# Kernel tuning notes

Hardware: AMD Instinct MI355X
Metric: run time of the kernel (lower is better)

The kernel has to match this reference:

```python
import jax, jax.numpy as jnp
import numpy as np


def setup_inputs() -> dict:
    key = jax.random.key(0)
    ks = jax.random.split(key, 5)
    B, T, I, H = 64, 512, 1024, 1024
    s = 1.0 / np.sqrt(H)
    return {
        "x": jax.random.normal(ks[0], (B, T, I), dtype=jnp.float32),
        "w_ih": jax.random.normal(ks[1], (4 * H, I), dtype=jnp.float32) * s,
        "b_ih": jax.random.normal(ks[2], (4 * H,), dtype=jnp.float32) * s,
        "w_hh": jax.random.normal(ks[3], (4 * H, H), dtype=jnp.float32) * s,
        "b_hh": jax.random.normal(ks[4], (4 * H,), dtype=jnp.float32) * s,
    }


def _lstm(x, w_ih, b_ih, w_hh, b_hh):
    B, T, _ = x.shape
    H = w_hh.shape[1]
    # Precompute input projections for all timesteps: [T, B, 4H]
    gx = jnp.einsum("bti,gi->tbg", x, w_ih) + b_ih
    h0 = jnp.zeros((B, H), dtype=x.dtype)
    c0 = jnp.zeros((B, H), dtype=x.dtype)

    def step(carry, g_x):
        h, c = carry
        gates = g_x + h @ w_hh.T + b_hh  # [B, 4H]
        i_lin, f_lin, g_lin, o_lin = jnp.split(gates, 4, axis=-1)
        i = jax.nn.sigmoid(i_lin)
        f = jax.nn.sigmoid(f_lin)
        g = jnp.tanh(g_lin)
        o = jax.nn.sigmoid(o_lin)
        c = f * c + i * g
        h = o * jnp.tanh(c)
        return (h, c), h

    (hT, cT), hs = jax.lax.scan(step, (h0, c0), gx)
    output = jnp.transpose(hs, (1, 0, 2))  # [B, T, H]
    hn = hT[None, :, :]  # [1, B, H]
    cn = cT[None, :, :]
    return output, hn, cn


def reference(x, w_ih, b_ih, w_hh, b_hh):
    return _lstm(x, w_ih, b_ih, w_hh, b_hh)
```

## Files before the change

kernel.cpp:

```cpp
#include <hip/hip_runtime.h>
#include <hip/hip_bf16.h>

#define Bv 64
#define Tv 512
#define Iv 1024
#define Hv 1024
#define G4v 4096
#define BH (Bv * Hv)
#define NHB 64
#define NXB 128
#define NBLK (NHB + NXB)
#define DEPTH 8
#define FSTR 16

typedef __attribute__((ext_vector_type(8))) short bf16x8;
typedef __attribute__((ext_vector_type(4))) float f32x4;

#define LOADC(p)    __hip_atomic_load((p), __ATOMIC_RELAXED, __HIP_MEMORY_SCOPE_AGENT)
#define STOREC(p,v) __hip_atomic_store((p), (v), __ATOMIC_RELAXED, __HIP_MEMORY_SCOPE_AGENT)

__device__ __forceinline__ float sigmoid_f(float v) { return 1.f / (1.f + __expf(-v)); }
__device__ __forceinline__ float tanh_f(float v) { return 1.f - 2.f / (__expf(2.f * v) + 1.f); }

__global__ void prep(const float* __restrict__ w_ih, const float* __restrict__ w_hh,
                     const float* __restrict__ b_ih, const float* __restrict__ b_hh,
                     __hip_bfloat16* __restrict__ wbih, __hip_bfloat16* __restrict__ wbhh,
                     float* __restrict__ bias, __hip_bfloat16* __restrict__ hbuf,
                     unsigned* __restrict__ hflag, unsigned* __restrict__ xflag) {
  unsigned i = blockIdx.x * 256u + threadIdx.x;
  wbih[i] = __float2bfloat16(w_ih[i]);
  wbhh[i] = __float2bfloat16(w_hh[i]);
  if (i < (unsigned)G4v) bias[i] = b_ih[i] + b_hh[i];
  if (i < 2u * BH) hbuf[i] = __float2bfloat16(0.f);
  if (i < (unsigned)(NHB * FSTR)) hflag[i] = 0u;
  if (i < (unsigned)(NXB * FSTR)) xflag[i] = 0u;
}

#define LOAD4(buf, cc)                                                  \
  _Pragma("unroll")                                                     \
  for (int j = 0; j < 4; ++j) {                                         \
    buf[2 * j]     = LOADC(hq + ((cc) * 4 + j) * 8);                    \
    buf[2 * j + 1] = LOADC(hq + ((cc) * 4 + j) * 8 + 1);                \
  }
#define MFMA4(buf, cc)                                                  \
  _Pragma("unroll")                                                     \
  for (int j = 0; j < 4; ++j) {                                         \
    int k0 = (((cc) * 4 + j) << 5) + lk;                                \
    union { unsigned long long q[2]; bf16x8 v; } ua;                    \
    ua.q[0] = buf[2 * j]; ua.q[1] = buf[2 * j + 1];                     \
    _Pragma("unroll")                                                   \
    for (int nf = 0; nf < 4; ++nf) {                                    \
      int n = nf * 16 + lrow;                                           \
      unsigned byt = (unsigned)((n << 11) + (k0 << 1)) ^ ((unsigned)(n & 7) << 4); \
      bf16x8 b = *(const bf16x8*)(&lds[byt]);                           \
      acc[nf] = __builtin_amdgcn_mfma_f32_16x16x32_bf16(ua.v, b, acc[nf], 0, 0, 0); \
    }                                                                   \
  }

__global__ void __launch_bounds__(256, 1) lstm_main(
    const float* __restrict__ x,
    const __hip_bfloat16* __restrict__ wbih,
    const __hip_bfloat16* __restrict__ wbhh,
    const float* __restrict__ bias,
    __hip_bfloat16* __restrict__ hbuf,
    float* __restrict__ xg,
    float* __restrict__ out,
    unsigned* __restrict__ hflag,
    unsigned* __restrict__ xflag,
    int ring)
{
  extern __shared__ char lds[];
  float* gbuf = (float*)(lds + 131072);

  const int bid  = blockIdx.x;
  const bool is_h = (bid < NHB);
  const int tid  = threadIdx.x;
  const int lane = tid & 63;
  const int wave = tid >> 6;
  const int lrow = lane & 15;
  const int lkg  = lane >> 4;
  const int lk   = lkg * 8;

  const int wg = is_h ? bid : ((bid - NHB) >> 1);
  const int rh = is_h ? 0 : ((bid - NHB) & 1);

  {
    const __hip_bfloat16* wsrc = is_h ? wbhh : wbih;
    for (int c = tid; c < 8192; c += 256) {
      int n   = c >> 7;
      int k16 = c & 127;
      int gc  = ((n >> 4) << 10) + (wg << 4) + (n & 15);
      uint4 v = *(const uint4*)(wsrc + ((size_t)gc << 10) + (k16 << 3));
      unsigned byt = (unsigned)((n << 11) + (k16 << 4)) ^ ((unsigned)(n & 7) << 4);
      *(uint4*)(&lds[byt]) = v;
    }
  }
  __syncthreads();

  if (!is_h) {
    const int j  = bid - NHB;
    const int wr = wave & 1;
    const int wc = wave >> 1;
    const int arow = rh * 32 + wr * 16 + lrow;
    const float* xa = x + (size_t)arow * (Tv * Iv) + lk;

    for (int t = 0; t < Tv; ++t) {
      if (t >= DEPTH) {
        if (wave == 0) {
          const unsigned tgt = (unsigned)(t - DEPTH + 1);
          for (;;) {
            unsigned hf = LOADC(&hflag[lane * FSTR]);
            if (__all(hf >= tgt)) break;
            __builtin_amdgcn_s_sleep(4);
          }
        }
        __syncthreads();
        asm volatile("" ::: "memory");
      }
      f32x4 acc[2];
      acc[0] = f32x4{0.f,0.f,0.f,0.f}; acc[1] = f32x4{0.f,0.f,0.f,0.f};
      const float* xt = xa + (size_t)t * Iv;
      #pragma unroll 4
      for (int ks = 0; ks < 32; ++ks) {
        int k0 = (ks << 5) + lk;
        float4 f0 = *(const float4*)(xt + (ks << 5));
        float4 f1 = *(const float4*)(xt + (ks << 5) + 4);
        union { __hip_bfloat16 e[8]; bf16x8 v; } u;
        u.e[0] = __float2bfloat16(f0.x); u.e[1] = __float2bfloat16(f0.y);
        u.e[2] = __float2bfloat16(f0.z); u.e[3] = __float2bfloat16(f0.w);
        u.e[4] = __float2bfloat16(f1.x); u.e[5] = __float2bfloat16(f1.y);
        u.e[6] = __float2bfloat16(f1.z); u.e[7] = __float2bfloat16(f1.w);
        bf16x8 b0, b1;
        {
          int n = wc * 32 + lrow;
          unsigned byt = (unsigned)((n << 11) + (k0 << 1)) ^ ((unsigned)(n & 7) << 4);
          b0 = *(const bf16x8*)(&lds[byt]);
          n += 16;
          byt = (unsigned)((n << 11) + (k0 << 1)) ^ ((unsigned)(n & 7) << 4);
          b1 = *(const bf16x8*)(&lds[byt]);
        }
        acc[0] = __builtin_amdgcn_mfma_f32_16x16x32_bf16(u.v, b0, acc[0], 0, 0, 0);
        acc[1] = __builtin_amdgcn_mfma_f32_16x16x32_bf16(u.v, b1, acc[1], 0, 0, 0);
      }
      float* dst = xg + (size_t)(t & (DEPTH - 1)) * (Bv * G4v);
      for (int nf = 0; nf < 2; ++nf) {
        int gc  = (wc * 2 + nf) * 1024 + (wg << 4) + lrow;
        int row = rh * 32 + wr * 16 + (lkg << 2);
        for (int r = 0; r < 4; ++r)
          STOREC(&dst[(size_t)(row + r) * G4v + gc], acc[nf][r]);
      }
      asm volatile("s_waitcnt vmcnt(0)" ::: "memory");
      __syncthreads();
      if (tid == 0) STOREC(&xflag[j * FSTR], (unsigned)(t + 1));
      __syncthreads();
    }
    return;
  }

  const int eb  = tid >> 2;
  const int ec0 = (tid & 3) << 2;
  float c_state[4] = {0.f, 0.f, 0.f, 0.f};
  float biasv[16];
  for (int g = 0; g < 4; ++g)
    for (int jj = 0; jj < 4; ++jj)
      biasv[g * 4 + jj] = bias[(g << 10) + (wg << 4) + ec0 + jj];

  const int ar = wave * 16 + lrow;

  for (int t = 0; t < Tv; ++t) {
    if (wave == 0) {
      const unsigned ht = (unsigned)t, xtg = (unsigned)(t + 1);
      const unsigned* xf = &xflag[(2 * wg + (lane & 1)) * FSTR];
      for (;;) {
        unsigned hf = LOADC(&hflag[lane * FSTR]);
        unsigned xv = LOADC(xf);
        if (__all(hf >= ht && xv >= xtg)) break;
        __builtin_amdgcn_s_sleep(1);
      }
    }
    __syncthreads();
    asm volatile("" ::: "memory");
    float xgv[16];
    {
      const unsigned long long* xq = (const unsigned long long*)
          (xg + (size_t)(t & (DEPTH - 1)) * (Bv * G4v) + (size_t)eb * G4v + (wg << 4) + ec0);
      #pragma unroll
      for (int g = 0; g < 4; ++g) {
        union { unsigned long long q[2]; float f[4]; } ux;
        ux.q[0] = LOADC(xq + g * 512);
        ux.q[1] = LOADC(xq + g * 512 + 1);
        xgv[g * 4 + 0] = ux.f[0]; xgv[g * 4 + 1] = ux.f[1];
        xgv[g * 4 + 2] = ux.f[2]; xgv[g * 4 + 3] = ux.f[3];
      }
    }
    f32x4 acc[4];
    for (int nf = 0; nf < 4; ++nf) acc[nf] = f32x4{0.f,0.f,0.f,0.f};
    if (ring) {
      const __hip_bfloat16* hp2 = hbuf + (size_t)t * BH;
      const char* hrow = (const char*)hp2 + ((size_t)ar << 11) + (lkg << 4);
      bf16x8 aqv[32];
      #pragma unroll
      for (int ks = 0; ks < 32; ++ks)
        aqv[ks] = *(const bf16x8*)(hrow + (ks << 6));
      #pragma unroll
      for (int ks = 0; ks < 32; ++ks) {
        int k0 = (ks << 5) + lk;
        #pragma unroll
        for (int nf = 0; nf < 4; ++nf) {
          int n = nf * 16 + lrow;
          unsigned byt = (unsigned)((n << 11) + (k0 << 1)) ^ ((unsigned)(n & 7) << 4);
          bf16x8 b = *(const bf16x8*)(&lds[byt]);
          acc[nf] = __builtin_amdgcn_mfma_f32_16x16x32_bf16(aqv[ks], b, acc[nf], 0, 0, 0);
        }
      }
    } else {
      const __hip_bfloat16* hp = hbuf + (size_t)((t + 1) & 1) * BH;
      const unsigned long long* hq = (const unsigned long long*)hp + (size_t)ar * 256 + lkg * 2;
      unsigned long long aqA[8], aqB[8];
      LOAD4(aqA, 0)
      LOAD4(aqB, 1)
      MFMA4(aqA, 0) LOAD4(aqA, 2)
      MFMA4(aqB, 1) LOAD4(aqB, 3)
      MFMA4(aqA, 2) LOAD4(aqA, 4)
      MFMA4(aqB, 3) LOAD4(aqB, 5)
      MFMA4(aqA, 4) LOAD4(aqA, 6)
      MFMA4(aqB, 5) LOAD4(aqB, 7)
      MFMA4(aqA, 6)
      MFMA4(aqB, 7)
    }
    #pragma unroll
    for (int nf = 0; nf < 4; ++nf)
      for (int r = 0; r < 4; ++r)
        gbuf[(wave * 16 + (lkg << 2) + r) * 65 + nf * 16 + lrow] = acc[nf][r];
    __syncthreads();
    float hv[4];
    #pragma unroll
    for (int jj = 0; jj < 4; ++jj) {
      int cc = ec0 + jj;
      float g0 = gbuf[eb * 65 +      cc] + xgv[0 + jj]  + biasv[0 + jj];
      float g1 = gbuf[eb * 65 + 16 + cc] + xgv[4 + jj]  + biasv[4 + jj];
      float g2 = gbuf[eb * 65 + 32 + cc] + xgv[8 + jj]  + biasv[8 + jj];
      float g3 = gbuf[eb * 65 + 48 + cc] + xgv[12 + jj] + biasv[12 + jj];
      float ig = sigmoid_f(g0);
      float fg = sigmoid_f(g1);
      float gg = tanh_f(g2);
      float og = sigmoid_f(g3);
      float cv = fg * c_state[jj] + ig * gg;
      c_state[jj] = cv;
      hv[jj] = og * tanh_f(cv);
    }
    __hip_bfloat16* hw = hbuf
        + (ring ? (size_t)(t + 1) * BH : (size_t)(t & 1) * BH)
        + ((size_t)eb << 10) + (wg << 4) + ec0;
    union { __hip_bfloat16 h[4]; unsigned long long q; } hu;
    for (int jj = 0; jj < 4; ++jj) hu.h[jj] = __float2bfloat16(hv[jj]);
    STOREC((unsigned long long*)hw, hu.q);
    asm volatile("s_waitcnt vmcnt(0)" ::: "memory");
    __syncthreads();
    if (tid == 0) STOREC(&hflag[wg * FSTR], (unsigned)(t + 1));
    float* ow = out + (size_t)eb * (Tv * Hv) + ((size_t)t << 10) + (wg << 4) + ec0;
    f32x4 ov = {hv[0], hv[1], hv[2], hv[3]};
    __builtin_nontemporal_store(ov, (f32x4*)ow);
    if (t == Tv - 1) {
      float* hn = out + (size_t)Bv * Tv * Hv + ((size_t)eb << 10) + (wg << 4) + ec0;
      float* cn = hn + (size_t)Bv * Hv;
      for (int jj = 0; jj < 4; ++jj) { hn[jj] = hv[jj]; cn[jj] = c_state[jj]; }
    }
    __syncthreads();
  }
}

extern "C" void kernel_launch(void* const* d_in, const int* in_sizes, int n_in,
                              void* d_out, int out_size, void* d_ws, size_t ws_size,
                              hipStream_t stream) {
  const float* x    = (const float*)d_in[0];
  const float* w_ih = (const float*)d_in[1];
  const float* b_ih = (const float*)d_in[2];
  const float* w_hh = (const float*)d_in[3];
  const float* b_hh = (const float*)d_in[4];
  float* out = (float*)d_out;

  char* ws = (char*)d_ws;
  __hip_bfloat16* wbih = (__hip_bfloat16*)(ws);
  __hip_bfloat16* wbhh = (__hip_bfloat16*)(ws + ((size_t)8 << 20));
  float*          bias = (float*)(ws + ((size_t)16 << 20));
  float*          xg   = (float*)(ws + ((size_t)18 << 20));
  unsigned*       hflag= (unsigned*)(ws + ((size_t)26 << 20));
  unsigned*       xflag= (unsigned*)(ws + ((size_t)26 << 20) + 8192);

  const size_t ringBytes = (size_t)(Tv + 1) * BH * 2;
  const size_t needRing  = ((size_t)32 << 20) + ringBytes;
  const int ring = (ws_size >= needRing) ? 1 : 0;
  __hip_bfloat16* hbuf = ring
      ? (__hip_bfloat16*)(ws + ((size_t)32 << 20))
      : (__hip_bfloat16*)(ws + ((size_t)16 << 20) + 65536);

  hipLaunchKernelGGL(prep, dim3(16384), dim3(256), 0, stream,
                     w_ih, w_hh, b_ih, b_hh, wbih, wbhh, bias, hbuf, hflag, xflag);

  const unsigned ldsBytes = 131072u + 64u * 65u * 4u;
  hipFuncSetAttribute((const void*)lstm_main,
                      hipFuncAttributeMaxDynamicSharedMemorySize, (int)ldsBytes);

  const float* xA = x;
  const __hip_bfloat16* wbihA = wbih;
  const __hip_bfloat16* wbhhA = wbhh;
  const float* biasA = bias;
  __hip_bfloat16* hbufA = hbuf;
  float* xgA = xg;
  float* outA = out;
  unsigned* hflagA = hflag;
  unsigned* xflagA = xflag;
  int ringA = ring;
  void* args[10] = {(void*)&xA, (void*)&wbihA, (void*)&wbhhA, (void*)&biasA,
                    (void*)&hbufA, (void*)&xgA, (void*)&outA, (void*)&hflagA,
                    (void*)&xflagA, (void*)&ringA};

  hipError_t lerr = hipLaunchCooperativeKernel((const void*)lstm_main, dim3(NBLK),
                                               dim3(256), args, ldsBytes, stream);
  if (lerr != hipSuccess) {
    (void)hipGetLastError();
    hipLaunchKernelGGL(lstm_main, dim3(NBLK), dim3(256), ldsBytes, stream,
                       xA, wbihA, wbhhA, biasA, hbufA, xgA, outA, hflagA, xflagA, ringA);
  }
}
```

Measured before the change: 4.597 ms.

## Split recurrent batch into two half-batches with independent step flags

Each recurrent block now processes the 64-row batch as two 32-row halves sequentially per timestep, each with its own set of completion flags. Blocks can start the next step's first half once all blocks finish that half, letting halves overlap across the grid and hiding barrier latency. It doubles the number of grid-wide flag waits and block barriers per step, halves MFMA work per wave per phase, and replaces vectorised nontemporal output stores with scalar stores.

```diff
diff --git a/kernel.cpp b/kernel.cpp
--- a/kernel.cpp
+++ b/kernel.cpp
@@ -7,6 +7,7 @@
 #define Hv 1024
 #define G4v 4096
 #define BH (Bv * Hv)
+#define SB 32
 #define NHB 64
 #define NXB 128
 #define NBLK (NHB + NXB)
@@ -32,30 +33,9 @@
   wbhh[i] = __float2bfloat16(w_hh[i]);
   if (i < (unsigned)G4v) bias[i] = b_ih[i] + b_hh[i];
   if (i < 2u * BH) hbuf[i] = __float2bfloat16(0.f);
-  if (i < (unsigned)(NHB * FSTR)) hflag[i] = 0u;
+  if (i < (unsigned)(2 * NHB * FSTR)) hflag[i] = 0u;
   if (i < (unsigned)(NXB * FSTR)) xflag[i] = 0u;
 }
-
-#define LOAD4(buf, cc)                                                  \
-  _Pragma("unroll")                                                     \
-  for (int j = 0; j < 4; ++j) {                                         \
-    buf[2 * j]     = LOADC(hq + ((cc) * 4 + j) * 8);                    \
-    buf[2 * j + 1] = LOADC(hq + ((cc) * 4 + j) * 8 + 1);                \
-  }
-#define MFMA4(buf, cc)                                                  \
-  _Pragma("unroll")                                                     \
-  for (int j = 0; j < 4; ++j) {                                         \
-    int k0 = (((cc) * 4 + j) << 5) + lk;                                \
-    union { unsigned long long q[2]; bf16x8 v; } ua;                    \
-    ua.q[0] = buf[2 * j]; ua.q[1] = buf[2 * j + 1];                     \
-    _Pragma("unroll")                                                   \
-    for (int nf = 0; nf < 4; ++nf) {                                    \
-      int n = nf * 16 + lrow;                                           \
-      unsigned byt = (unsigned)((n << 11) + (k0 << 1)) ^ ((unsigned)(n & 7) << 4); \
-      bf16x8 b = *(const bf16x8*)(&lds[byt]);                           \
-      acc[nf] = __builtin_amdgcn_mfma_f32_16x16x32_bf16(ua.v, b, acc[nf], 0, 0, 0); \
-    }                                                                   \
-  }
 
 __global__ void __launch_bounds__(256, 1) lstm_main(
     const float* __restrict__ x,
@@ -109,8 +89,9 @@
         if (wave == 0) {
           const unsigned tgt = (unsigned)(t - DEPTH + 1);
           for (;;) {
-            unsigned hf = LOADC(&hflag[lane * FSTR]);
-            if (__all(hf >= tgt)) break;
+            unsigned a = LOADC(&hflag[lane * FSTR]);
+            unsigned b = LOADC(&hflag[(64 + lane) * FSTR]);
+            if (__all(a >= tgt && b >= tgt)) break;
             __builtin_amdgcn_s_sleep(4);
           }
         }
@@ -157,116 +138,129 @@
     return;
   }
 
-  const int eb  = tid >> 2;
-  const int ec0 = (tid & 3) << 2;
-  float c_state[4] = {0.f, 0.f, 0.f, 0.f};
-  float biasv[16];
+  const int wm  = wave >> 1;
+  const int wn  = wave & 1;
+  const int er  = tid >> 3;
+  const int ecl = (tid & 7) << 1;
+  float c_state[2][2] = {{0.f,0.f},{0.f,0.f}};
+  float biasv[8];
   for (int g = 0; g < 4; ++g)
-    for (int jj = 0; jj < 4; ++jj)
-      biasv[g * 4 + jj] = bias[(g << 10) + (wg << 4) + ec0 + jj];
-
-  const int ar = wave * 16 + lrow;
+    for (int jj = 0; jj < 2; ++jj)
+      biasv[g * 2 + jj] = bias[(g << 10) + (wg << 4) + ecl + jj];
 
   for (int t = 0; t < Tv; ++t) {
-    if (wave == 0) {
-      const unsigned ht = (unsigned)t, xtg = (unsigned)(t + 1);
-      const unsigned* xf = &xflag[(2 * wg + (lane & 1)) * FSTR];
-      for (;;) {
-        unsigned hf = LOADC(&hflag[lane * FSTR]);
-        unsigned xv = LOADC(xf);
-        if (__all(hf >= ht && xv >= xtg)) break;
-        __builtin_amdgcn_s_sleep(1);
-      }
+    #pragma unroll
+    for (int S = 0; S < 2; ++S) {
+      if (wave == 0) {
+        const unsigned* xf = &xflag[(2 * wg + (lane & 1)) * FSTR];
+        for (;;) {
+          unsigned hf = LOADC(&hflag[(S * 64 + lane) * FSTR]);
+          bool ok = (hf >= (unsigned)t);
+          if (S == 0) { unsigned xv = LOADC(xf); ok = ok && (xv >= (unsigned)(t + 1)); }
+          if (__all(ok)) break;
+          __builtin_amdgcn_s_sleep(1);
+        }
+      }
+      __syncthreads();
+      asm volatile("" ::: "memory");
+      float xgv[8];
+      {
+        const float* xgs = xg + (size_t)(t & (DEPTH - 1)) * (Bv * G4v)
+                         + (size_t)(S * SB + er) * G4v + (wg << 4) + ecl;
+        #pragma unroll
+        for (int g = 0; g < 4; ++g) {
+          union { unsigned long long q; float f[2]; } ux;
+          ux.q = LOADC((const unsigned long long*)(xgs + (g << 10)));
+          xgv[g * 2 + 0] = ux.f[0]; xgv[g * 2 + 1] = ux.f[1];
+        }
+      }
+      const int ar = S * SB + wm * 16 + lrow;
+      f32x4 acc[2];
+      acc[0] = f32x4{0.f,0.f,0.f,0.f}; acc[1] = f32x4{0.f,0.f,0.f,0.f};
+      if (ring) {
+        const char* hrow = (const char*)(hbuf + (size_t)t * BH) + ((size_t)ar << 11) + (lkg << 4);
+        bf16x8 aqv[32];
+        #pragma unroll
+        for (int ks = 0; ks < 32; ++ks)
+          aqv[ks] = *(const bf16x8*)(hrow + (ks << 6));
+        #pragma unroll
+        for (int ks = 0; ks < 32; ++ks) {
+          int k0 = (ks << 5) + lk;
+          #pragma unroll
+          for (int nfl = 0; nfl < 2; ++nfl) {
+            int n = (wn * 2 + nfl) * 16 + lrow;
+            unsigned byt = (unsigned)((n << 11) + (k0 << 1)) ^ ((unsigned)(n & 7) << 4);
+            bf16x8 b = *(const bf16x8*)(&lds[byt]);
+            acc[nfl] = __builtin_amdgcn_mfma_f32_16x16x32_bf16(aqv[ks], b, acc[nfl], 0, 0, 0);
+          }
+        }
+      } else {
+        const unsigned long long* hq = (const unsigned long long*)
+            (hbuf + (size_t)(t & 1) * BH) + (size_t)ar * 256 + lkg * 2;
+        bf16x8 aqv[32];
+        #pragma unroll
+        for (int ks = 0; ks < 32; ++ks) {
+          union { unsigned long long q[2]; bf16x8 v; } ua;
+          ua.q[0] = LOADC(hq + ks * 8);
+          ua.q[1] = LOADC(hq + ks * 8 + 1);
+          aqv[ks] = ua.v;
+        }
+        #pragma unroll
+        for (int ks = 0; ks < 32; ++ks) {
+          int k0 = (ks << 5) + lk;
+          #pragma unroll
+          for (int nfl = 0; nfl < 2; ++nfl) {
+            int n = (wn * 2 + nfl) * 16 + lrow;
+            unsigned byt = (unsigned)((n << 11) + (k0 << 1)) ^ ((unsigned)(n & 7) << 4);
+            bf16x8 b = *(const bf16x8*)(&lds[byt]);
+            acc[nfl] = __builtin_amdgcn_mfma_f32_16x16x32_bf16(aqv[ks], b, acc[nfl], 0, 0, 0);
+          }
+        }
+      }
+      #pragma unroll
+      for (int nfl = 0; nfl < 2; ++nfl)
+        for (int r = 0; r < 4; ++r)
+          gbuf[(wm * 16 + (lkg << 2) + r) * 65 + (wn * 2 + nfl) * 16 + lrow] = acc[nfl][r];
+      __syncthreads();
+      float hv[2];
+      #pragma unroll
+      for (int jj = 0; jj < 2; ++jj) {
+        int cc = ecl + jj;
+        float g0 = gbuf[er * 65 +      cc] + xgv[0 + jj] + biasv[0 + jj];
+        float g1 = gbuf[er * 65 + 16 + cc] + xgv[2 + jj] + biasv[2 + jj];
+        float g2 = gbuf[er * 65 + 32 + cc] + xgv[4 + jj] + biasv[4 + jj];
+        float g3 = gbuf[er * 65 + 48 + cc] + xgv[6 + jj] + biasv[6 + jj];
+        float ig = sigmoid_f(g0);
+        float fg = sigmoid_f(g1);
+        float gg = tanh_f(g2);
+        float og = sigmoid_f(g3);
+        float cv = fg * c_state[S][jj] + ig * gg;
+        c_state[S][jj] = cv;
+        hv[jj] = og * tanh_f(cv);
+      }
+      {
+        __hip_bfloat16* hw = hbuf
+            + (ring ? (size_t)(t + 1) * BH : (size_t)((t + 1) & 1) * BH)
+            + ((size_t)(S * SB + er) << 10) + (wg << 4) + ecl;
+        union { __hip_bfloat16 h[2]; unsigned u; } hu;
+        hu.h[0] = __float2bfloat16(hv[0]); hu.h[1] = __float2bfloat16(hv[1]);
+        STOREC((unsigned*)hw, hu.u);
+      }
+      asm volatile("s_waitcnt vmcnt(0)" ::: "memory");
+      __syncthreads();
+      if (tid == 0) STOREC(&hflag[(S * 64 + wg) * FSTR], (unsigned)(t + 1));
+      {
+        float* ow = out + (size_t)(S * SB + er) * (Tv * Hv) + ((size_t)t << 10) + (wg << 4) + ecl;
+        ow[0] = hv[0]; ow[1] = hv[1];
+        if (t == Tv - 1) {
+          float* hn = out + (size_t)Bv * Tv * Hv + ((size_t)(S * SB + er) << 10) + (wg << 4) + ecl;
+          float* cn = hn + (size_t)BH;
+          hn[0] = hv[0]; hn[1] = hv[1];
+          cn[0] = c_state[S][0]; cn[1] = c_state[S][1];
+        }
+      }
+      __syncthreads();
     }
-    __syncthreads();
-    asm volatile("" ::: "memory");
-    float xgv[16];
-    {
-      const unsigned long long* xq = (const unsigned long long*)
-          (xg + (size_t)(t & (DEPTH - 1)) * (Bv * G4v) + (size_t)eb * G4v + (wg << 4) + ec0);
-      #pragma unroll
-      for (int g = 0; g < 4; ++g) {
-        union { unsigned long long q[2]; float f[4]; } ux;
-        ux.q[0] = LOADC(xq + g * 512);
-        ux.q[1] = LOADC(xq + g * 512 + 1);
-        xgv[g * 4 + 0] = ux.f[0]; xgv[g * 4 + 1] = ux.f[1];
-        xgv[g * 4 + 2] = ux.f[2]; xgv[g * 4 + 3] = ux.f[3];
-      }
-    }
-    f32x4 acc[4];
-    for (int nf = 0; nf < 4; ++nf) acc[nf] = f32x4{0.f,0.f,0.f,0.f};
-    if (ring) {
-      const __hip_bfloat16* hp2 = hbuf + (size_t)t * BH;
-      const char* hrow = (const char*)hp2 + ((size_t)ar << 11) + (lkg << 4);
-      bf16x8 aqv[32];
-      #pragma unroll
-      for (int ks = 0; ks < 32; ++ks)
-        aqv[ks] = *(const bf16x8*)(hrow + (ks << 6));
-      #pragma unroll
-      for (int ks = 0; ks < 32; ++ks) {
-        int k0 = (ks << 5) + lk;
-        #pragma unroll
-        for (int nf = 0; nf < 4; ++nf) {
-          int n = nf * 16 + lrow;
-          unsigned byt = (unsigned)((n << 11) + (k0 << 1)) ^ ((unsigned)(n & 7) << 4);
-          bf16x8 b = *(const bf16x8*)(&lds[byt]);
-          acc[nf] = __builtin_amdgcn_mfma_f32_16x16x32_bf16(aqv[ks], b, acc[nf], 0, 0, 0);
-        }
-      }
-    } else {
-      const __hip_bfloat16* hp = hbuf + (size_t)((t + 1) & 1) * BH;
-      const unsigned long long* hq = (const unsigned long long*)hp + (size_t)ar * 256 + lkg * 2;
-      unsigned long long aqA[8], aqB[8];
-      LOAD4(aqA, 0)
-      LOAD4(aqB, 1)
-      MFMA4(aqA, 0) LOAD4(aqA, 2)
-      MFMA4(aqB, 1) LOAD4(aqB, 3)
-      MFMA4(aqA, 2) LOAD4(aqA, 4)
-      MFMA4(aqB, 3) LOAD4(aqB, 5)
-      MFMA4(aqA, 4) LOAD4(aqA, 6)
-      MFMA4(aqB, 5) LOAD4(aqB, 7)
-      MFMA4(aqA, 6)
-      MFMA4(aqB, 7)
-    }
-    #pragma unroll
-    for (int nf = 0; nf < 4; ++nf)
-      for (int r = 0; r < 4; ++r)
-        gbuf[(wave * 16 + (lkg << 2) + r) * 65 + nf * 16 + lrow] = acc[nf][r];
-    __syncthreads();
-    float hv[4];
-    #pragma unroll
-    for (int jj = 0; jj < 4; ++jj) {
-      int cc = ec0 + jj;
-      float g0 = gbuf[eb * 65 +      cc] + xgv[0 + jj]  + biasv[0 + jj];
-      float g1 = gbuf[eb * 65 + 16 + cc] + xgv[4 + jj]  + biasv[4 + jj];
-      float g2 = gbuf[eb * 65 + 32 + cc] + xgv[8 + jj]  + biasv[8 + jj];
-      float g3 = gbuf[eb * 65 + 48 + cc] + xgv[12 + jj] + biasv[12 + jj];
-      float ig = sigmoid_f(g0);
-      float fg = sigmoid_f(g1);
-      float gg = tanh_f(g2);
-      float og = sigmoid_f(g3);
-      float cv = fg * c_state[jj] + ig * gg;
-      c_state[jj] = cv;
-      hv[jj] = og * tanh_f(cv);
-    }
-    __hip_bfloat16* hw = hbuf
-        + (ring ? (size_t)(t + 1) * BH : (size_t)(t & 1) * BH)
-        + ((size_t)eb << 10) + (wg << 4) + ec0;
-    union { __hip_bfloat16 h[4]; unsigned long long q; } hu;
-    for (int jj = 0; jj < 4; ++jj) hu.h[jj] = __float2bfloat16(hv[jj]);
-    STOREC((unsigned long long*)hw, hu.q);
-    asm volatile("s_waitcnt vmcnt(0)" ::: "memory");
-    __syncthreads();
-    if (tid == 0) STOREC(&hflag[wg * FSTR], (unsigned)(t + 1));
-    float* ow = out + (size_t)eb * (Tv * Hv) + ((size_t)t << 10) + (wg << 4) + ec0;
-    f32x4 ov = {hv[0], hv[1], hv[2], hv[3]};
-    __builtin_nontemporal_store(ov, (f32x4*)ow);
-    if (t == Tv - 1) {
-      float* hn = out + (size_t)Bv * Tv * Hv + ((size_t)eb << 10) + (wg << 4) + ec0;
-      float* cn = hn + (size_t)Bv * Hv;
-      for (int jj = 0; jj < 4; ++jj) { hn[jj] = hv[jj]; cn[jj] = c_state[jj]; }
-    }
-    __syncthreads();
   }
 }
 
@@ -298,7 +292,7 @@
   hipLaunchKernelGGL(prep, dim3(16384), dim3(256), 0, stream,
                      w_ih, w_hh, b_ih, b_hh, wbih, wbhh, bias, hbuf, hflag, xflag);
 
-  const unsigned ldsBytes = 131072u + 64u * 65u * 4u;
+  const unsigned ldsBytes = 131072u + 32u * 65u * 4u;
   hipFuncSetAttribute((const void*)lstm_main,
                       hipFuncAttributeMaxDynamicSharedMemorySize, (int)ldsBytes);
 
```

New measurement: 6.822 ms. 48.4% more time.

## Apply LSTM gate epilogue directly in MFMA accumulator layout, drop LDS staging

Applied to the files above, without the earlier changes.

The recurrent step now computes gate nonlinearities straight from the MFMA accumulator registers instead of staging results through an LDS gate buffer. This removes one __syncthreads, the trailing barrier and the LDS round-trip. The cost is scalar, strided stores of h (bf16 short stores with sc1) and output, and strided xg loads in place of vectorized ones. The non-ring path is also simplified to load all h fragments up front, and its double-buffer parity is flipped.

```diff
diff --git a/kernel.cpp b/kernel.cpp
--- a/kernel.cpp
+++ b/kernel.cpp
@@ -21,6 +21,10 @@
 
 __device__ __forceinline__ float sigmoid_f(float v) { return 1.f / (1.f + __expf(-v)); }
 __device__ __forceinline__ float tanh_f(float v) { return 1.f - 2.f / (__expf(2.f * v) + 1.f); }
+
+__device__ __forceinline__ void store_short_sc1(void* p, unsigned short v) {
+  asm volatile("global_store_short %0, %1, off sc1" :: "v"(p), "v"((unsigned)v) : "memory");
+}
 
 __global__ void prep(const float* __restrict__ w_ih, const float* __restrict__ w_hh,
                      const float* __restrict__ b_ih, const float* __restrict__ b_hh,
@@ -35,27 +39,6 @@
   if (i < (unsigned)(NHB * FSTR)) hflag[i] = 0u;
   if (i < (unsigned)(NXB * FSTR)) xflag[i] = 0u;
 }
-
-#define LOAD4(buf, cc)                                                  \
-  _Pragma("unroll")                                                     \
-  for (int j = 0; j < 4; ++j) {                                         \
-    buf[2 * j]     = LOADC(hq + ((cc) * 4 + j) * 8);                    \
-    buf[2 * j + 1] = LOADC(hq + ((cc) * 4 + j) * 8 + 1);                \
-  }
-#define MFMA4(buf, cc)                                                  \
-  _Pragma("unroll")                                                     \
-  for (int j = 0; j < 4; ++j) {                                         \
-    int k0 = (((cc) * 4 + j) << 5) + lk;                                \
-    union { unsigned long long q[2]; bf16x8 v; } ua;                    \
-    ua.q[0] = buf[2 * j]; ua.q[1] = buf[2 * j + 1];                     \
-    _Pragma("unroll")                                                   \
-    for (int nf = 0; nf < 4; ++nf) {                                    \
-      int n = nf * 16 + lrow;                                           \
-      unsigned byt = (unsigned)((n << 11) + (k0 << 1)) ^ ((unsigned)(n & 7) << 4); \
-      bf16x8 b = *(const bf16x8*)(&lds[byt]);                           \
-      acc[nf] = __builtin_amdgcn_mfma_f32_16x16x32_bf16(ua.v, b, acc[nf], 0, 0, 0); \
-    }                                                                   \
-  }
 
 __global__ void __launch_bounds__(256, 1) lstm_main(
     const float* __restrict__ x,
@@ -70,7 +53,6 @@
     int ring)
 {
   extern __shared__ char lds[];
-  float* gbuf = (float*)(lds + 131072);
 
   const int bid  = blockIdx.x;
   const bool is_h = (bid < NHB);
@@ -157,13 +139,12 @@
     return;
   }
 
-  const int eb  = tid >> 2;
-  const int ec0 = (tid & 3) << 2;
+  const int orow0 = wave * 16 + (lkg << 2);
+  const int ocol  = (wg << 4) + lrow;
   float c_state[4] = {0.f, 0.f, 0.f, 0.f};
-  float biasv[16];
-  for (int g = 0; g < 4; ++g)
-    for (int jj = 0; jj < 4; ++jj)
-      biasv[g * 4 + jj] = bias[(g << 10) + (wg << 4) + ec0 + jj];
+  float biasv[4];
+  #pragma unroll
+  for (int g = 0; g < 4; ++g) biasv[g] = bias[(g << 10) + ocol];
 
   const int ar = wave * 16 + lrow;
 
@@ -180,93 +161,85 @@
     }
     __syncthreads();
     asm volatile("" ::: "memory");
+    f32x4 acc[4];
+    for (int nf = 0; nf < 4; ++nf) acc[nf] = f32x4{0.f,0.f,0.f,0.f};
+    bf16x8 aqv[32];
+    const unsigned long long* hq = nullptr;
+    if (ring) {
+      const char* hrow = (const char*)(hbuf + (size_t)t * BH) + ((size_t)ar << 11) + (lkg << 4);
+      #pragma unroll
+      for (int ks = 0; ks < 32; ++ks)
+        aqv[ks] = *(const bf16x8*)(hrow + (ks << 6));
+    } else {
+      hq = (const unsigned long long*)(hbuf + (size_t)(t & 1) * BH) + (size_t)ar * 256 + lkg * 2;
+      #pragma unroll
+      for (int ks = 0; ks < 32; ++ks) {
+        union { unsigned long long q[2]; bf16x8 v; } ua;
+        ua.q[0] = LOADC(hq + ks * 8);
+        ua.q[1] = LOADC(hq + ks * 8 + 1);
+        aqv[ks] = ua.v;
+      }
+    }
     float xgv[16];
     {
-      const unsigned long long* xq = (const unsigned long long*)
-          (xg + (size_t)(t & (DEPTH - 1)) * (Bv * G4v) + (size_t)eb * G4v + (wg << 4) + ec0);
-      #pragma unroll
-      for (int g = 0; g < 4; ++g) {
-        union { unsigned long long q[2]; float f[4]; } ux;
-        ux.q[0] = LOADC(xq + g * 512);
-        ux.q[1] = LOADC(xq + g * 512 + 1);
-        xgv[g * 4 + 0] = ux.f[0]; xgv[g * 4 + 1] = ux.f[1];
-        xgv[g * 4 + 2] = ux.f[2]; xgv[g * 4 + 3] = ux.f[3];
-      }
-    }
-    f32x4 acc[4];
-    for (int nf = 0; nf < 4; ++nf) acc[nf] = f32x4{0.f,0.f,0.f,0.f};
-    if (ring) {
-      const __hip_bfloat16* hp2 = hbuf + (size_t)t * BH;
-      const char* hrow = (const char*)hp2 + ((size_t)ar << 11) + (lkg << 4);
-      bf16x8 aqv[32];
-      #pragma unroll
-      for (int ks = 0; ks < 32; ++ks)
-        aqv[ks] = *(const bf16x8*)(hrow + (ks << 6));
-      #pragma unroll
-      for (int ks = 0; ks < 32; ++ks) {
-        int k0 = (ks << 5) + lk;
+      const float* xgs = xg + (size_t)(t & (DEPTH - 1)) * (Bv * G4v);
+      #pragma unroll
+      for (int g = 0; g < 4; ++g)
         #pragma unroll
-        for (int nf = 0; nf < 4; ++nf) {
-          int n = nf * 16 + lrow;
-          unsigned byt = (unsigned)((n << 11) + (k0 << 1)) ^ ((unsigned)(n & 7) << 4);
-          bf16x8 b = *(const bf16x8*)(&lds[byt]);
-          acc[nf] = __builtin_amdgcn_mfma_f32_16x16x32_bf16(aqv[ks], b, acc[nf], 0, 0, 0);
-        }
-      }
-    } else {
-      const __hip_bfloat16* hp = hbuf + (size_t)((t + 1) & 1) * BH;
-      const unsigned long long* hq = (const unsigned long long*)hp + (size_t)ar * 256 + lkg * 2;
-      unsigned long long aqA[8], aqB[8];
-      LOAD4(aqA, 0)
-      LOAD4(aqB, 1)
-      MFMA4(aqA, 0) LOAD4(aqA, 2)
-      MFMA4(aqB, 1) LOAD4(aqB, 3)
-      MFMA4(aqA, 2) LOAD4(aqA, 4)
-      MFMA4(aqB, 3) LOAD4(aqB, 5)
-      MFMA4(aqA, 4) LOAD4(aqA, 6)
-      MFMA4(aqB, 5) LOAD4(aqB, 7)
-      MFMA4(aqA, 6)
-      MFMA4(aqB, 7)
+        for (int r = 0; r < 4; ++r)
+          xgv[g * 4 + r] = LOADC(xgs + (size_t)(orow0 + r) * G4v + (g << 10) + ocol);
     }
     #pragma unroll
-    for (int nf = 0; nf < 4; ++nf)
-      for (int r = 0; r < 4; ++r)
-        gbuf[(wave * 16 + (lkg << 2) + r) * 65 + nf * 16 + lrow] = acc[nf][r];
-    __syncthreads();
+    for (int ks = 0; ks < 32; ++ks) {
+      int k0 = (ks << 5) + lk;
+      #pragma unroll
+      for (int nf = 0; nf < 4; ++nf) {
+        int n = nf * 16 + lrow;
+        unsigned byt = (unsigned)((n << 11) + (k0 << 1)) ^ ((unsigned)(n & 7) << 4);
+        bf16x8 b = *(const bf16x8*)(&lds[byt]);
+        acc[nf] = __builtin_amdgcn_mfma_f32_16x16x32_bf16(aqv[ks], b, acc[nf], 0, 0, 0);
+      }
+    }
     float hv[4];
     #pragma unroll
-    for (int jj = 0; jj < 4; ++jj) {
-      int cc = ec0 + jj;
-      float g0 = gbuf[eb * 65 +      cc] + xgv[0 + jj]  + biasv[0 + jj];
-      float g1 = gbuf[eb * 65 + 16 + cc] + xgv[4 + jj]  + biasv[4 + jj];
-      float g2 = gbuf[eb * 65 + 32 + cc] + xgv[8 + jj]  + biasv[8 + jj];
-      float g3 = gbuf[eb * 65 + 48 + cc] + xgv[12 + jj] + biasv[12 + jj];
+    for (int r = 0; r < 4; ++r) {
+      float g0 = acc[0][r] + xgv[0 + r]  + biasv[0];
+      float g1 = acc[1][r] + xgv[4 + r]  + biasv[1];
+      float g2 = acc[2][r] + xgv[8 + r]  + biasv[2];
+      float g3 = acc[3][r] + xgv[12 + r] + biasv[3];
       float ig = sigmoid_f(g0);
       float fg = sigmoid_f(g1);
       float gg = tanh_f(g2);
       float og = sigmoid_f(g3);
-      float cv = fg * c_state[jj] + ig * gg;
-      c_state[jj] = cv;
-      hv[jj] = og * tanh_f(cv);
-    }
-    __hip_bfloat16* hw = hbuf
-        + (ring ? (size_t)(t + 1) * BH : (size_t)(t & 1) * BH)
-        + ((size_t)eb << 10) + (wg << 4) + ec0;
-    union { __hip_bfloat16 h[4]; unsigned long long q; } hu;
-    for (int jj = 0; jj < 4; ++jj) hu.h[jj] = __float2bfloat16(hv[jj]);
-    STOREC((unsigned long long*)hw, hu.q);
+      float cv = fg * c_state[r] + ig * gg;
+      c_state[r] = cv;
+      hv[r] = og * tanh_f(cv);
+    }
+    {
+      __hip_bfloat16* hs = hbuf
+          + (ring ? (size_t)(t + 1) * BH : (size_t)((t + 1) & 1) * BH) + ocol;
+      #pragma unroll
+      for (int r = 0; r < 4; ++r) {
+        __hip_bfloat16 hb = __float2bfloat16(hv[r]);
+        store_short_sc1(hs + ((size_t)(orow0 + r) << 10), *(unsigned short*)&hb);
+      }
+    }
     asm volatile("s_waitcnt vmcnt(0)" ::: "memory");
     __syncthreads();
     if (tid == 0) STOREC(&hflag[wg * FSTR], (unsigned)(t + 1));
-    float* ow = out + (size_t)eb * (Tv * Hv) + ((size_t)t << 10) + (wg << 4) + ec0;
-    f32x4 ov = {hv[0], hv[1], hv[2], hv[3]};
-    __builtin_nontemporal_store(ov, (f32x4*)ow);
+    #pragma unroll
+    for (int r = 0; r < 4; ++r) {
+      float* ow = out + (size_t)(orow0 + r) * (Tv * Hv) + ((size_t)t << 10) + ocol;
+      __builtin_nontemporal_store(hv[r], ow);
+    }
     if (t == Tv - 1) {
-      float* hn = out + (size_t)Bv * Tv * Hv + ((size_t)eb << 10) + (wg << 4) + ec0;
-      float* cn = hn + (size_t)Bv * Hv;
-      for (int jj = 0; jj < 4; ++jj) { hn[jj] = hv[jj]; cn[jj] = c_state[jj]; }
-    }
-    __syncthreads();
+      #pragma unroll
+      for (int r = 0; r < 4; ++r) {
+        float* hn = out + (size_t)Bv * Tv * Hv + ((size_t)(orow0 + r) << 10) + ocol;
+        __builtin_nontemporal_store(hv[r], hn);
+        __builtin_nontemporal_store(c_state[r], hn + BH);
+      }
+    }
   }
 }
 
@@ -298,7 +271,7 @@
   hipLaunchKernelGGL(prep, dim3(16384), dim3(256), 0, stream,
                      w_ih, w_hh, b_ih, b_hh, wbih, wbhh, bias, hbuf, hflag, xflag);
 
-  const unsigned ldsBytes = 131072u + 64u * 65u * 4u;
+  const unsigned ldsBytes = 131072u;
   hipFuncSetAttribute((const void*)lstm_main,
                       hipFuncAttributeMaxDynamicSharedMemorySize, (int)ldsBytes);
 
```

New measurement: 4.732 ms. 1.03x slower.
